# Kernel tuning notes

Hardware: AMD Instinct MI355X
Metric: run time of the kernel (lower is better)

Reference implementation:

```python
import jax, jax.numpy as jnp
import numpy as np

# 3D PGA grade slices over the 16-component multivector (contiguous in standard basis order)
GRADE_SLICES = [(0, 1), (1, 5), (5, 11), (11, 15), (15, 16)]
GRADE_DIMS = [1, 4, 6, 4, 1]


def setup_inputs() -> dict:
    key = jax.random.key(0)
    ks = jax.random.split(key, 11)
    x = jax.random.normal(ks[0], (8, 2048, 128, 16), dtype=jnp.float32)
    inp = {"x": x}
    for g, d in enumerate(GRADE_DIMS):
        # match nn.Linear default init scale ~ U(-1/sqrt(d), 1/sqrt(d)); randn is fine for a numeric baseline
        inp[f"w{g}"] = jax.random.normal(ks[1 + 2 * g], (d, d), dtype=jnp.float32) / np.sqrt(d)
        inp[f"b{g}"] = jax.random.normal(ks[2 + 2 * g], (d,), dtype=jnp.float32) / np.sqrt(d)
    return inp


def reference(x, w0, b0, w1, b1, w2, b2, w3, b3, w4, b4):
    ws = [w0, w1, w2, w3, w4]
    bs = [b0, b1, b2, b3, b4]
    # Block-diagonal per-grade linear: gather slice, y = x_g @ W_g^T + b_g, scatter back.
    # Since grade index sets are contiguous, scatter == concatenate along last dim.
    outs = []
    for (lo, hi), w, b in zip(GRADE_SLICES, ws, bs):
        xg = x[..., lo:hi]                       # [..., d_g]
        outs.append(jnp.einsum("...i,oi->...o", xg, w) + b)
    return jnp.concatenate(outs, axis=-1)        # [..., 16]
```

## Files before the change

kernel.cpp:

```cpp
#include <hip/hip_runtime.h>


__global__ __launch_bounds__(256) void GradeWiseLinear_kernel(
    const float* __restrict__ x,
    const float* __restrict__ w0, const float* __restrict__ b0,
    const float* __restrict__ w1, const float* __restrict__ b1,
    const float* __restrict__ w2, const float* __restrict__ b2,
    const float* __restrict__ w3, const float* __restrict__ b3,
    const float* __restrict__ w4, const float* __restrict__ b4,
    float* __restrict__ out, int nrows)
{
    __shared__ float s[86];
    {
        int t = threadIdx.x;
        if (t < 86) {
            float v;
            if      (t == 0)  v = w0[0];
            else if (t < 17)  v = w1[t - 1];
            else if (t < 53)  v = w2[t - 17];
            else if (t < 69)  v = w3[t - 53];
            else if (t == 69) v = w4[0];
            else if (t == 70) v = b0[0];
            else if (t < 75)  v = b1[t - 71];
            else if (t < 81)  v = b2[t - 75];
            else if (t < 85)  v = b3[t - 81];
            else              v = b4[0];
            s[t] = v;
        }
    }
    __syncthreads();

    int r = blockIdx.x * 256 + threadIdx.x;
    if (r >= nrows) return;

    const float4* __restrict__ x4 = (const float4*)x;
    float4* __restrict__ o4 = (float4*)out;
    const int base = r * 4;

    float4 a = x4[base + 0];
    float4 p = x4[base + 1];
    float4 c = x4[base + 2];
    float4 d = x4[base + 3];

    float4 y0, y1, y2, y3;

    y0.x = s[70] + s[0] * a.x;

    y0.y = s[71] + s[1]  * a.y + s[2]  * a.z + s[3]  * a.w + s[4]  * p.x;
    y0.z = s[72] + s[5]  * a.y + s[6]  * a.z + s[7]  * a.w + s[8]  * p.x;
    y0.w = s[73] + s[9]  * a.y + s[10] * a.z + s[11] * a.w + s[12] * p.x;
    y1.x = s[74] + s[13] * a.y + s[14] * a.z + s[15] * a.w + s[16] * p.x;

    y1.y = s[75] + s[17] * p.y + s[18] * p.z + s[19] * p.w
                 + s[20] * c.x + s[21] * c.y + s[22] * c.z;
    y1.z = s[76] + s[23] * p.y + s[24] * p.z + s[25] * p.w
                 + s[26] * c.x + s[27] * c.y + s[28] * c.z;
    y1.w = s[77] + s[29] * p.y + s[30] * p.z + s[31] * p.w
                 + s[32] * c.x + s[33] * c.y + s[34] * c.z;
    y2.x = s[78] + s[35] * p.y + s[36] * p.z + s[37] * p.w
                 + s[38] * c.x + s[39] * c.y + s[40] * c.z;
    y2.y = s[79] + s[41] * p.y + s[42] * p.z + s[43] * p.w
                 + s[44] * c.x + s[45] * c.y + s[46] * c.z;
    y2.z = s[80] + s[47] * p.y + s[48] * p.z + s[49] * p.w
                 + s[50] * c.x + s[51] * c.y + s[52] * c.z;

    y2.w = s[81] + s[53] * c.w + s[54] * d.x + s[55] * d.y + s[56] * d.z;
    y3.x = s[82] + s[57] * c.w + s[58] * d.x + s[59] * d.y + s[60] * d.z;
    y3.y = s[83] + s[61] * c.w + s[62] * d.x + s[63] * d.y + s[64] * d.z;
    y3.z = s[84] + s[65] * c.w + s[66] * d.x + s[67] * d.y + s[68] * d.z;

    y3.w = s[85] + s[69] * d.w;

    o4[base + 0] = y0;
    o4[base + 1] = y1;
    o4[base + 2] = y2;
    o4[base + 3] = y3;
}

extern "C" void kernel_launch(void* const* d_in, const int* in_sizes, int n_in,
                              void* d_out, int out_size, void* d_ws, size_t ws_size,
                              hipStream_t stream) {
    const float* x  = (const float*)d_in[0];
    const float* w0 = (const float*)d_in[1];
    const float* b0 = (const float*)d_in[2];
    const float* w1 = (const float*)d_in[3];
    const float* b1 = (const float*)d_in[4];
    const float* w2 = (const float*)d_in[5];
    const float* b2 = (const float*)d_in[6];
    const float* w3 = (const float*)d_in[7];
    const float* b3 = (const float*)d_in[8];
    const float* w4 = (const float*)d_in[9];
    const float* b4 = (const float*)d_in[10];
    float* out = (float*)d_out;

    int nrows = in_sizes[0] / 16;
    int block = 256;
    int grid = (nrows + block - 1) / block;

    GradeWiseLinear_kernel<<<grid, block, 0, stream>>>(
        x, w0, b0, w1, b1, w2, b2, w3, b3, w4, b4, out, nrows);
}
```

Before: 252.8 us.

## Stage row tiles through swizzled LDS for fully coalesced global loads and stores

Each block now loads 1024 consecutive float4s with unit-stride per-thread indexing into a swizzled shared-memory tile, then each thread reads its row's four float4s from LDS, computes, and writes results back through the tile before coalesced global stores. This replaces the strided 64-byte-per-thread float4 accesses, which split each wavefront's request across many cache lines. The XOR swizzle is meant to avoid LDS bank conflicts. It adds two barriers and 16 KB of LDS per block, which may limit occupancy, and it drops the tail bounds check, so the row count must be a multiple of 256.

```diff
diff --git a/kernel.cpp b/kernel.cpp
--- a/kernel.cpp
+++ b/kernel.cpp
@@ -8,9 +8,11 @@
     const float* __restrict__ w2, const float* __restrict__ b2,
     const float* __restrict__ w3, const float* __restrict__ b3,
     const float* __restrict__ w4, const float* __restrict__ b4,
-    float* __restrict__ out, int nrows)
+    float* __restrict__ out, int n4)
 {
     __shared__ float s[86];
+    __shared__ float4 tile[1024];
+
     {
         int t = threadIdx.x;
         if (t < 86) {
@@ -28,40 +30,54 @@
             s[t] = v;
         }
     }
-    __syncthreads();
 
-    int r = blockIdx.x * 256 + threadIdx.x;
-    if (r >= nrows) return;
+    const int t = threadIdx.x;
+    const int blockBase = blockIdx.x * 1024;
+    if (blockBase >= n4) return;
 
     const float4* __restrict__ x4 = (const float4*)x;
     float4* __restrict__ o4 = (float4*)out;
-    const int base = r * 4;
 
-    float4 a = x4[base + 0];
-    float4 p = x4[base + 1];
-    float4 c = x4[base + 2];
-    float4 d = x4[base + 3];
+    const int pm1 = ((t >> 2) ^ (t >> 4)) & 3;
+    const int phys_t = (t & ~3) | ((t & 3) ^ pm1);
+
+    float4 i0 = x4[blockBase + t];
+    float4 i1 = x4[blockBase + t + 256];
+    float4 i2 = x4[blockBase + t + 512];
+    float4 i3 = x4[blockBase + t + 768];
+    tile[phys_t      ] = i0;
+    tile[phys_t + 256] = i1;
+    tile[phys_t + 512] = i2;
+    tile[phys_t + 768] = i3;
+    __syncthreads();
+
+    const int pm2 = (t ^ (t >> 2)) & 3;
+    const int rb  = t * 4;
+    float4 a = tile[rb + (pm2 ^ 0)];
+    float4 q = tile[rb + (pm2 ^ 1)];
+    float4 c = tile[rb + (pm2 ^ 2)];
+    float4 d = tile[rb + (pm2 ^ 3)];
 
     float4 y0, y1, y2, y3;
 
     y0.x = s[70] + s[0] * a.x;
 
-    y0.y = s[71] + s[1]  * a.y + s[2]  * a.z + s[3]  * a.w + s[4]  * p.x;
-    y0.z = s[72] + s[5]  * a.y + s[6]  * a.z + s[7]  * a.w + s[8]  * p.x;
-    y0.w = s[73] + s[9]  * a.y + s[10] * a.z + s[11] * a.w + s[12] * p.x;
-    y1.x = s[74] + s[13] * a.y + s[14] * a.z + s[15] * a.w + s[16] * p.x;
+    y0.y = s[71] + s[1]  * a.y + s[2]  * a.z + s[3]  * a.w + s[4]  * q.x;
+    y0.z = s[72] + s[5]  * a.y + s[6]  * a.z + s[7]  * a.w + s[8]  * q.x;
+    y0.w = s[73] + s[9]  * a.y + s[10] * a.z + s[11] * a.w + s[12] * q.x;
+    y1.x = s[74] + s[13] * a.y + s[14] * a.z + s[15] * a.w + s[16] * q.x;
 
-    y1.y = s[75] + s[17] * p.y + s[18] * p.z + s[19] * p.w
+    y1.y = s[75] + s[17] * q.y + s[18] * q.z + s[19] * q.w
                  + s[20] * c.x + s[21] * c.y + s[22] * c.z;
-    y1.z = s[76] + s[23] * p.y + s[24] * p.z + s[25] * p.w
+    y1.z = s[76] + s[23] * q.y + s[24] * q.z + s[25] * q.w
                  + s[26] * c.x + s[27] * c.y + s[28] * c.z;
-    y1.w = s[77] + s[29] * p.y + s[30] * p.z + s[31] * p.w
+    y1.w = s[77] + s[29] * q.y + s[30] * q.z + s[31] * q.w
                  + s[32] * c.x + s[33] * c.y + s[34] * c.z;
-    y2.x = s[78] + s[35] * p.y + s[36] * p.z + s[37] * p.w
+    y2.x = s[78] + s[35] * q.y + s[36] * q.z + s[37] * q.w
                  + s[38] * c.x + s[39] * c.y + s[40] * c.z;
-    y2.y = s[79] + s[41] * p.y + s[42] * p.z + s[43] * p.w
+    y2.y = s[79] + s[41] * q.y + s[42] * q.z + s[43] * q.w
                  + s[44] * c.x + s[45] * c.y + s[46] * c.z;
-    y2.z = s[80] + s[47] * p.y + s[48] * p.z + s[49] * p.w
+    y2.z = s[80] + s[47] * q.y + s[48] * q.z + s[49] * q.w
                  + s[50] * c.x + s[51] * c.y + s[52] * c.z;
 
     y2.w = s[81] + s[53] * c.w + s[54] * d.x + s[55] * d.y + s[56] * d.z;
@@ -71,10 +87,16 @@
 
     y3.w = s[85] + s[69] * d.w;
 
-    o4[base + 0] = y0;
-    o4[base + 1] = y1;
-    o4[base + 2] = y2;
-    o4[base + 3] = y3;
+    tile[rb + (pm2 ^ 0)] = y0;
+    tile[rb + (pm2 ^ 1)] = y1;
+    tile[rb + (pm2 ^ 2)] = y2;
+    tile[rb + (pm2 ^ 3)] = y3;
+    __syncthreads();
+
+    o4[blockBase + t      ] = tile[phys_t];
+    o4[blockBase + t + 256] = tile[phys_t + 256];
+    o4[blockBase + t + 512] = tile[phys_t + 512];
+    o4[blockBase + t + 768] = tile[phys_t + 768];
 }
 
 extern "C" void kernel_launch(void* const* d_in, const int* in_sizes, int n_in,
@@ -93,10 +115,10 @@
     const float* b4 = (const float*)d_in[10];
     float* out = (float*)d_out;
 
-    int nrows = in_sizes[0] / 16;
+    int n4 = in_sizes[0] / 4;
     int block = 256;
-    int grid = (nrows + block - 1) / block;
+    int grid = (n4 + 1023) / 1024;
 
     GradeWiseLinear_kernel<<<grid, block, 0, stream>>>(
-        x, w0, b0, w1, b1, w2, b2, w3, b3, w4, b4, out, nrows);
+        x, w0, b0, w1, b1, w2, b2, w3, b3, w4, b4, out, n4);
 }
```

Result: no change. 249.0 us (-1.5%).
